# Performance work log

Hardware: AMD Instinct MI355X
Metric: run time of the kernel (lower is better)

## Reference

```python
import jax, jax.numpy as jnp
import numpy as np

B, T, C, D = 16, 2048, 1024, 64

def setup_inputs() -> dict:
    key = jax.random.key(0)
    kx, kq, kk, kv = jax.random.split(key, 4)
    x = jax.random.normal(kx, (B, T, C), dtype=jnp.float32)
    # nn.Linear(emb_size, head_size, bias=False): y = x @ W, store W as [C, D]
    s = 1.0 / np.sqrt(C)
    Wq = jax.random.normal(kq, (C, D), dtype=jnp.float32) * s
    Wk = jax.random.normal(kk, (C, D), dtype=jnp.float32) * s
    Wv = jax.random.normal(kv, (C, D), dtype=jnp.float32) * s
    return {"x": x, "Wq": Wq, "Wk": Wk, "Wv": Wv}

def reference(x, Wq, Wk, Wv):
    Bv, Tv, Cv = x.shape
    q = jnp.einsum('btc,cd->btd', x, Wq)
    k = jnp.einsum('btc,cd->btd', x, Wk)
    v = jnp.einsum('btc,cd->btd', x, Wv)
    # NOTE: original scales by C**0.5 (emb_size), not head_size**0.5
    scores = jnp.einsum('bqd,bkd->bqk', q, k) / jnp.sqrt(jnp.float32(Cv))
    causal = jnp.tril(jnp.ones((Tv, Tv), dtype=bool))
    scores = jnp.where(causal[None, :, :], scores, -jnp.inf)
    weights = jax.nn.softmax(scores, axis=-1)
    # dropout(p=0.4) omitted: reference assumes eval mode (identity)
    return jnp.einsum('bqk,bkd->bqd', weights, v)
```

## Files before the change

### kernel.cpp

```cpp
#include <hip/hip_runtime.h>
#include <math.h>


#define B_ 16
#define T_ 2048
#define C_ 1024
#define D_ 64
#define BT_ (B_ * T_)

typedef __attribute__((ext_vector_type(8))) short short8;
typedef __attribute__((ext_vector_type(4))) float f32x4;

__device__ __forceinline__ unsigned short f2bf(float f) {
    unsigned u = __float_as_uint(f);
    return (unsigned short)((u + 0x7fffu + ((u >> 16) & 1u)) >> 16);
}
__device__ __forceinline__ float bf2f(unsigned short h) {
    return __uint_as_float(((unsigned)h) << 16);
}
#define MFMA16(a, b, c) __builtin_amdgcn_mfma_f32_16x16x32_bf16((a), (b), (c), 0, 0, 0)

__global__ __launch_bounds__(256) void wprep_kernel(
    const float* __restrict__ Wq, const float* __restrict__ Wk,
    const float* __restrict__ Wv, short* __restrict__ WTh, short* __restrict__ WTl)
{
    int id = blockIdx.x * 256 + threadIdx.x;
    int n  = id >> 6;
    int c0 = (id & 63) << 4;
    const float* W = (n < 64) ? Wq : (n < 128) ? Wk : Wv;
    int d = n & 63;
    short8 h0, h1, l0, l1;
    #pragma unroll
    for (int i = 0; i < 8; ++i) {
        float w = W[(size_t)(c0 + i) * 64 + d];
        unsigned short hh = f2bf(w);
        h0[i] = (short)hh; l0[i] = (short)f2bf(w - bf2f(hh));
        float w2 = W[(size_t)(c0 + 8 + i) * 64 + d];
        unsigned short hh2 = f2bf(w2);
        h1[i] = (short)hh2; l1[i] = (short)f2bf(w2 - bf2f(hh2));
    }
    size_t o = (size_t)n * 1024 + c0;
    *(short8*)&WTh[o] = h0; *(short8*)&WTh[o + 8] = h1;
    *(short8*)&WTl[o] = l0; *(short8*)&WTl[o + 8] = l1;
}

__global__ __launch_bounds__(256) void qkv_mfma_kernel(
    const float* __restrict__ x, const short* __restrict__ WTh,
    const short* __restrict__ WTl, float* __restrict__ qf,
    short* __restrict__ kbf, short* __restrict__ vtb)
{
    __shared__ alignas(16) short xh[64 * 64];
    __shared__ alignas(16) short xl[64 * 64];

    const int tid = threadIdx.x;
    const int row0 = blockIdx.x * 64;
    const int lane = tid & 63, w = tid >> 6;
    const int lr = lane & 15, lg = lane >> 4;
    const int sr = tid >> 2, sc = (tid & 3) * 16;

    f32x4 acc[4][3];
    #pragma unroll
    for (int mt = 0; mt < 4; ++mt)
        #pragma unroll
        for (int gi = 0; gi < 3; ++gi) acc[mt][gi] = (f32x4){0.f, 0.f, 0.f, 0.f};

    for (int kb = 0; kb < C_; kb += 64) {
        float xv[16];
        const float* xp = &x[(size_t)(row0 + sr) * C_ + kb + sc];
        *(float4*)&xv[0]  = *(const float4*)&xp[0];
        *(float4*)&xv[4]  = *(const float4*)&xp[4];
        *(float4*)&xv[8]  = *(const float4*)&xp[8];
        *(float4*)&xv[12] = *(const float4*)&xp[12];
        short8 h0, h1, l0, l1;
        #pragma unroll
        for (int i = 0; i < 8; ++i) {
            unsigned short hh = f2bf(xv[i]);
            h0[i] = (short)hh; l0[i] = (short)f2bf(xv[i] - bf2f(hh));
            unsigned short hh2 = f2bf(xv[8 + i]);
            h1[i] = (short)hh2; l1[i] = (short)f2bf(xv[8 + i] - bf2f(hh2));
        }
        __syncthreads();
        {
            int u0 = (sc >> 3), u1 = u0 + 1;
            *(short8*)&xh[sr * 64 + (u0 ^ (sr & 7)) * 8] = h0;
            *(short8*)&xh[sr * 64 + (u1 ^ (sr & 7)) * 8] = h1;
            *(short8*)&xl[sr * 64 + (u0 ^ (sr & 7)) * 8] = l0;
            *(short8*)&xl[sr * 64 + (u1 ^ (sr & 7)) * 8] = l1;
        }
        __syncthreads();

        #pragma unroll
        for (int kc = 0; kc < 2; ++kc) {
            short8 ah[4], al[4];
            #pragma unroll
            for (int mt = 0; mt < 4; ++mt) {
                int r = mt * 16 + lr;
                int usw = (kc * 4 + lg) ^ (r & 7);
                ah[mt] = *(short8*)&xh[r * 64 + usw * 8];
                al[mt] = *(short8*)&xl[r * 64 + usw * 8];
            }
            #pragma unroll
            for (int gi = 0; gi < 3; ++gi) {
                int n = (3 * w + gi) * 16 + lr;
                size_t wo = (size_t)n * 1024 + kb + kc * 32 + lg * 8;
                short8 wh = *(const short8*)&WTh[wo];
                short8 wl = *(const short8*)&WTl[wo];
                #pragma unroll
                for (int mt = 0; mt < 4; ++mt) {
                    acc[mt][gi] = MFMA16(ah[mt], wh, acc[mt][gi]);
                    acc[mt][gi] = MFMA16(ah[mt], wl, acc[mt][gi]);
                    acc[mt][gi] = MFMA16(al[mt], wh, acc[mt][gi]);
                }
            }
        }
    }

    #pragma unroll
    for (int mt = 0; mt < 4; ++mt) {
        int rbase = row0 + mt * 16 + lg * 4;
        #pragma unroll
        for (int gi = 0; gi < 3; ++gi) {
            int g = 3 * w + gi;
            f32x4 a = acc[mt][gi];
            int col = g * 16 + lr;
            if (g < 4) {
                #pragma unroll
                for (int reg = 0; reg < 4; ++reg)
                    qf[(size_t)(rbase + reg) * 64 + col] = a[reg];
            } else if (g < 8) {
                #pragma unroll
                for (int reg = 0; reg < 4; ++reg)
                    kbf[(size_t)(rbase + reg) * 64 + (col - 64)] = (short)f2bf(a[reg]);
            } else {
                int d = col - 128;
                int bb = rbase >> 11, t0 = rbase & (T_ - 1);
                short4 pk;
                pk.x = (short)f2bf(a[0]); pk.y = (short)f2bf(a[1]);
                pk.z = (short)f2bf(a[2]); pk.w = (short)f2bf(a[3]);
                *(short4*)&vtb[((size_t)(bb * 64 + d) << 11) + t0] = pk;
            }
        }
    }
}

__global__ __launch_bounds__(256) void attn_mfma_kernel(
    const float* __restrict__ qf, const short* __restrict__ kbf,
    const short* __restrict__ vtb, float* __restrict__ out)
{
    __shared__ alignas(16) short kbuf[64 * 64];
    __shared__ alignas(16) short vbuf[64 * 64];
    __shared__ alignas(16) short pbuf[4 * 16 * 64];

    const int bid = blockIdx.x;
    const int b  = bid & 15;
    const int qt = 31 - (bid >> 4);
    const int tid = threadIdx.x;
    const int lane = tid & 63, w = tid >> 6;
    const int lr = lane & 15, lg = lane >> 4;
    const int qrow0 = qt * 64 + w * 16;
    const size_t base_tok = (size_t)b * T_;

    short8 qh[2], ql[2];
    #pragma unroll
    for (int kc = 0; kc < 2; ++kc) {
        const float* qp = &qf[(base_tok + qrow0 + lr) * 64 + kc * 32 + lg * 8];
        float4 q0 = *(const float4*)qp;
        float4 q1 = *(const float4*)(qp + 4);
        float qs[8] = {q0.x, q0.y, q0.z, q0.w, q1.x, q1.y, q1.z, q1.w};
        #pragma unroll
        for (int i = 0; i < 8; ++i) {
            float v = qs[i] * 0.03125f;
            unsigned short hh = f2bf(v);
            qh[kc][i] = (short)hh;
            ql[kc][i] = (short)f2bf(v - bf2f(hh));
        }
    }

    f32x4 o[4];
    #pragma unroll
    for (int dt = 0; dt < 4; ++dt) o[dt] = (f32x4){0.f, 0.f, 0.f, 0.f};
    float m[4]    = {-INFINITY, -INFINITY, -INFINITY, -INFINITY};
    float lsum[4] = {0.f, 0.f, 0.f, 0.f};

    const int sr = tid >> 2, su = tid & 3;
    const short* Kb = kbf + base_tok * 64;
    const short* Vb = vtb + (size_t)b * 64 * T_;

    int4 kreg[2], vreg[2];
    auto load_regs = [&](int jt) {
        int j0 = jt * 64;
        #pragma unroll
        for (int c = 0; c < 2; ++c) {
            kreg[c] = *(const int4*)&Kb[(size_t)(j0 + sr) * 64 + (su * 2 + c) * 8];
            vreg[c] = *(const int4*)&Vb[(size_t)sr * T_ + j0 + (su * 2 + c) * 8];
        }
    };
    auto write_bufs = [&]() {
        #pragma unroll
        for (int c = 0; c < 2; ++c) {
            int usw = (su * 2 + c) ^ (sr & 7);
            *(int4*)&kbuf[sr * 64 + usw * 8] = kreg[c];
            *(int4*)&vbuf[sr * 64 + usw * 8] = vreg[c];
        }
    };

    load_regs(0);
    write_bufs();
    __syncthreads();

    for (int jt = 0; jt <= qt; ++jt) {
        if (jt < qt) load_regs(jt + 1);

        f32x4 s[4];
        #pragma unroll
        for (int nt = 0; nt < 4; ++nt) s[nt] = (f32x4){0.f, 0.f, 0.f, 0.f};
        #pragma unroll
        for (int kc = 0; kc < 2; ++kc)
            #pragma unroll
            for (int nt = 0; nt < 4; ++nt) {
                int kj = nt * 16 + lr;
                int usw = (kc * 4 + lg) ^ (kj & 7);
                short8 kf = *(short8*)&kbuf[kj * 64 + usw * 8];
                s[nt] = MFMA16(qh[kc], kf, s[nt]);
                s[nt] = MFMA16(ql[kc], kf, s[nt]);
            }

        if (jt == qt) {
            int j0 = jt * 64;
            #pragma unroll
            for (int nt = 0; nt < 4; ++nt) {
                int j = j0 + nt * 16 + lr;
                #pragma unroll
                for (int reg = 0; reg < 4; ++reg)
                    if (j > qrow0 + lg * 4 + reg) s[nt][reg] = -INFINITY;
            }
        }

        float corr[4], psum[4] = {0.f, 0.f, 0.f, 0.f};
        #pragma unroll
        for (int reg = 0; reg < 4; ++reg) {
            float vmax = fmaxf(fmaxf(s[0][reg], s[1][reg]),
                               fmaxf(s[2][reg], s[3][reg]));
            vmax = fmaxf(vmax, __shfl_xor(vmax, 1));
            vmax = fmaxf(vmax, __shfl_xor(vmax, 2));
            vmax = fmaxf(vmax, __shfl_xor(vmax, 4));
            vmax = fmaxf(vmax, __shfl_xor(vmax, 8));
            float mnew = fmaxf(m[reg], vmax);
            corr[reg] = __expf(m[reg] - mnew);
            m[reg] = mnew;
        }
        #pragma unroll
        for (int nt = 0; nt < 4; ++nt)
            #pragma unroll
            for (int reg = 0; reg < 4; ++reg) {
                float p = __expf(s[nt][reg] - m[reg]);
                psum[reg] += p;
                int qr = lg * 4 + reg;
                int colj = nt * 16 + lr;
                int usw = (colj >> 3) ^ (qr & 7);
                pbuf[(w * 16 + qr) * 64 + usw * 8 + (colj & 7)] = (short)f2bf(p);
            }
        #pragma unroll
        for (int reg = 0; reg < 4; ++reg)
            lsum[reg] = lsum[reg] * corr[reg] + psum[reg];
        #pragma unroll
        for (int dt = 0; dt < 4; ++dt) {
            o[dt][0] *= corr[0]; o[dt][1] *= corr[1];
            o[dt][2] *= corr[2]; o[dt][3] *= corr[3];
        }

        asm volatile("s_waitcnt lgkmcnt(0)" ::: "memory");
        __builtin_amdgcn_sched_barrier(0);
        short8 pf[2];
        #pragma unroll
        for (int kc = 0; kc < 2; ++kc) {
            int usw = (kc * 4 + lg) ^ (lr & 7);
            pf[kc] = *(short8*)&pbuf[(w * 16 + lr) * 64 + usw * 8];
        }
        #pragma unroll
        for (int dt = 0; dt < 4; ++dt)
            #pragma unroll
            for (int kc = 0; kc < 2; ++kc) {
                int d = dt * 16 + lr;
                int usw = (kc * 4 + lg) ^ (d & 7);
                short8 vf = *(short8*)&vbuf[d * 64 + usw * 8];
                o[dt] = MFMA16(pf[kc], vf, o[dt]);
            }

        if (jt < qt) {
            __syncthreads();
            write_bufs();
            __syncthreads();
        }
    }

    #pragma unroll
    for (int reg = 0; reg < 4; ++reg) {
        lsum[reg] += __shfl_xor(lsum[reg], 1);
        lsum[reg] += __shfl_xor(lsum[reg], 2);
        lsum[reg] += __shfl_xor(lsum[reg], 4);
        lsum[reg] += __shfl_xor(lsum[reg], 8);
        lsum[reg] = 1.f / lsum[reg];
    }
    #pragma unroll
    for (int dt = 0; dt < 4; ++dt)
        #pragma unroll
        for (int reg = 0; reg < 4; ++reg)
            out[(base_tok + qrow0 + lg * 4 + reg) * 64 + dt * 16 + lr] =
                o[dt][reg] * lsum[reg];
}

extern "C" void kernel_launch(void* const* d_in, const int* in_sizes, int n_in,
                              void* d_out, int out_size, void* d_ws, size_t ws_size,
                              hipStream_t stream) {
    const float* x  = (const float*)d_in[0];
    const float* Wq = (const float*)d_in[1];
    const float* Wk = (const float*)d_in[2];
    const float* Wv = (const float*)d_in[3];
    float* out = (float*)d_out;

    float* qf  = (float*)d_ws;
    short* kbf = (short*)(qf + (size_t)BT_ * 64);
    short* vtb = kbf + (size_t)BT_ * 64;
    short* WTh = vtb + (size_t)BT_ * 64;
    short* WTl = WTh + (size_t)192 * 1024;

    wprep_kernel<<<48, 256, 0, stream>>>(Wq, Wk, Wv, WTh, WTl);
    qkv_mfma_kernel<<<512, 256, 0, stream>>>(x, WTh, WTl, qf, kbf, vtb);
    attn_mfma_kernel<<<512, 256, 0, stream>>>(qf, kbf, vtb, out);
}
```

Measured before the change: 315.9 us.

## Rebalance attention per-wave causal tiles, halve QKV block rows, tile weight prep

The attention kernel now gives each wave its own 16-row query tile. Waves pair short and long causal rows so work is balanced, and each wave reads K and V fragments directly from global memory into registers with K double-buffered. This removes the shared K/V staging and the block-wide barriers. The QKV projection uses 32-row blocks (1024 blocks) to raise occupancy, and weight prep transposes through shared memory for coalesced loads. The trade-off is more redundant global/L2 traffic for K/V, since each wave reads the same data separately, plus more register pressure.

Measured after the change: 326.8 us. 1.03x slower.

```diff
diff --git a/kernel.cpp b/kernel.cpp
--- a/kernel.cpp
+++ b/kernel.cpp
@@ -24,22 +24,29 @@
     const float* __restrict__ Wq, const float* __restrict__ Wk,
     const float* __restrict__ Wv, short* __restrict__ WTh, short* __restrict__ WTl)
 {
-    int id = blockIdx.x * 256 + threadIdx.x;
-    int n  = id >> 6;
-    int c0 = (id & 63) << 4;
-    const float* W = (n < 64) ? Wq : (n < 128) ? Wk : Wv;
-    int d = n & 63;
+    __shared__ float ws[64][65];
+    const int bid = blockIdx.x, tid = threadIdx.x;
+    const int wi = bid >> 4, ct = bid & 15, c0 = ct * 64;
+    const float* W = (wi == 0) ? Wq : (wi == 1) ? Wk : Wv;
+    #pragma unroll
+    for (int i = 0; i < 4; ++i) {
+        int rr = (tid >> 4) + i * 16;
+        int dd = (tid & 15) * 4;
+        *(float4*)&ws[rr][dd] = *(const float4*)&W[(size_t)(c0 + rr) * 64 + dd];
+    }
+    __syncthreads();
+    const int d = tid >> 2, cc0 = (tid & 3) * 16;
     short8 h0, h1, l0, l1;
     #pragma unroll
     for (int i = 0; i < 8; ++i) {
-        float w = W[(size_t)(c0 + i) * 64 + d];
-        unsigned short hh = f2bf(w);
-        h0[i] = (short)hh; l0[i] = (short)f2bf(w - bf2f(hh));
-        float w2 = W[(size_t)(c0 + 8 + i) * 64 + d];
-        unsigned short hh2 = f2bf(w2);
-        h1[i] = (short)hh2; l1[i] = (short)f2bf(w2 - bf2f(hh2));
-    }
-    size_t o = (size_t)n * 1024 + c0;
+        float v = ws[cc0 + i][d];
+        unsigned short hh = f2bf(v);
+        h0[i] = (short)hh; l0[i] = (short)f2bf(v - bf2f(hh));
+        float v2 = ws[cc0 + 8 + i][d];
+        unsigned short hh2 = f2bf(v2);
+        h1[i] = (short)hh2; l1[i] = (short)f2bf(v2 - bf2f(hh2));
+    }
+    size_t o = (size_t)(wi * 64 + d) * 1024 + c0 + cc0;
     *(short8*)&WTh[o] = h0; *(short8*)&WTh[o + 8] = h1;
     *(short8*)&WTl[o] = l0; *(short8*)&WTl[o + 8] = l1;
 }
@@ -49,51 +56,45 @@
     const short* __restrict__ WTl, float* __restrict__ qf,
     short* __restrict__ kbf, short* __restrict__ vtb)
 {
-    __shared__ alignas(16) short xh[64 * 64];
-    __shared__ alignas(16) short xl[64 * 64];
+    __shared__ alignas(16) short xh[32 * 64];
+    __shared__ alignas(16) short xl[32 * 64];
 
     const int tid = threadIdx.x;
-    const int row0 = blockIdx.x * 64;
+    const int row0 = blockIdx.x * 32;
     const int lane = tid & 63, w = tid >> 6;
     const int lr = lane & 15, lg = lane >> 4;
-    const int sr = tid >> 2, sc = (tid & 3) * 16;
-
-    f32x4 acc[4][3];
-    #pragma unroll
-    for (int mt = 0; mt < 4; ++mt)
+    const int sr = tid >> 3, sc = (tid & 7) * 8;
+
+    f32x4 acc[2][3];
+    #pragma unroll
+    for (int mt = 0; mt < 2; ++mt)
         #pragma unroll
         for (int gi = 0; gi < 3; ++gi) acc[mt][gi] = (f32x4){0.f, 0.f, 0.f, 0.f};
 
     for (int kb = 0; kb < C_; kb += 64) {
-        float xv[16];
+        float xv[8];
         const float* xp = &x[(size_t)(row0 + sr) * C_ + kb + sc];
-        *(float4*)&xv[0]  = *(const float4*)&xp[0];
-        *(float4*)&xv[4]  = *(const float4*)&xp[4];
-        *(float4*)&xv[8]  = *(const float4*)&xp[8];
-        *(float4*)&xv[12] = *(const float4*)&xp[12];
-        short8 h0, h1, l0, l1;
+        *(float4*)&xv[0] = *(const float4*)&xp[0];
+        *(float4*)&xv[4] = *(const float4*)&xp[4];
+        short8 h0, l0;
         #pragma unroll
         for (int i = 0; i < 8; ++i) {
             unsigned short hh = f2bf(xv[i]);
             h0[i] = (short)hh; l0[i] = (short)f2bf(xv[i] - bf2f(hh));
-            unsigned short hh2 = f2bf(xv[8 + i]);
-            h1[i] = (short)hh2; l1[i] = (short)f2bf(xv[8 + i] - bf2f(hh2));
         }
         __syncthreads();
         {
-            int u0 = (sc >> 3), u1 = u0 + 1;
-            *(short8*)&xh[sr * 64 + (u0 ^ (sr & 7)) * 8] = h0;
-            *(short8*)&xh[sr * 64 + (u1 ^ (sr & 7)) * 8] = h1;
-            *(short8*)&xl[sr * 64 + (u0 ^ (sr & 7)) * 8] = l0;
-            *(short8*)&xl[sr * 64 + (u1 ^ (sr & 7)) * 8] = l1;
+            int u0 = (sc >> 3) ^ (sr & 7);
+            *(short8*)&xh[sr * 64 + u0 * 8] = h0;
+            *(short8*)&xl[sr * 64 + u0 * 8] = l0;
         }
         __syncthreads();
 
         #pragma unroll
         for (int kc = 0; kc < 2; ++kc) {
-            short8 ah[4], al[4];
-            #pragma unroll
-            for (int mt = 0; mt < 4; ++mt) {
+            short8 ah[2], al[2];
+            #pragma unroll
+            for (int mt = 0; mt < 2; ++mt) {
                 int r = mt * 16 + lr;
                 int usw = (kc * 4 + lg) ^ (r & 7);
                 ah[mt] = *(short8*)&xh[r * 64 + usw * 8];
@@ -106,7 +107,7 @@
                 short8 wh = *(const short8*)&WTh[wo];
                 short8 wl = *(const short8*)&WTl[wo];
                 #pragma unroll
-                for (int mt = 0; mt < 4; ++mt) {
+                for (int mt = 0; mt < 2; ++mt) {
                     acc[mt][gi] = MFMA16(ah[mt], wh, acc[mt][gi]);
                     acc[mt][gi] = MFMA16(ah[mt], wl, acc[mt][gi]);
                     acc[mt][gi] = MFMA16(al[mt], wh, acc[mt][gi]);
@@ -116,7 +117,7 @@
     }
 
     #pragma unroll
-    for (int mt = 0; mt < 4; ++mt) {
+    for (int mt = 0; mt < 2; ++mt) {
         int rbase = row0 + mt * 16 + lg * 4;
         #pragma unroll
         for (int gi = 0; gi < 3; ++gi) {
@@ -147,23 +148,31 @@
     const float* __restrict__ qf, const short* __restrict__ kbf,
     const short* __restrict__ vtb, float* __restrict__ out)
 {
-    __shared__ alignas(16) short kbuf[64 * 64];
-    __shared__ alignas(16) short vbuf[64 * 64];
     __shared__ alignas(16) short pbuf[4 * 16 * 64];
 
     const int bid = blockIdx.x;
     const int b  = bid & 15;
-    const int qt = 31 - (bid >> 4);
+    const int pp = (bid >> 4) & 31;
+    const int sw = (bid >> 8) & 1;
     const int tid = threadIdx.x;
     const int lane = tid & 63, w = tid >> 6;
     const int lr = lane & 15, lg = lane >> 4;
-    const int qrow0 = qt * 64 + w * 16;
+
+    const int sel = w >> 1;
+    const int hv  = (w & 1) ^ sw;
+    const int t   = hv ? (127 - 2 * pp - sel) : (2 * pp + sel);
+    const int trow0 = t * 16;
+    const int njt = (t >> 2) + 1;
+
     const size_t base_tok = (size_t)b * T_;
+    const short* Kb = kbf + base_tok * 64;
+    const short* Vb = vtb + (size_t)b * 64 * T_;
+    short* pw = pbuf + w * 16 * 64;
 
     short8 qh[2], ql[2];
     #pragma unroll
     for (int kc = 0; kc < 2; ++kc) {
-        const float* qp = &qf[(base_tok + qrow0 + lr) * 64 + kc * 32 + lg * 8];
+        const float* qp = &qf[(base_tok + trow0 + lr) * 64 + kc * 32 + lg * 8];
         float4 q0 = *(const float4*)qp;
         float4 q1 = *(const float4*)(qp + 4);
         float qs[8] = {q0.x, q0.y, q0.z, q0.w, q1.x, q1.y, q1.z, q1.w};
@@ -182,65 +191,54 @@
     float m[4]    = {-INFINITY, -INFINITY, -INFINITY, -INFINITY};
     float lsum[4] = {0.f, 0.f, 0.f, 0.f};
 
-    const int sr = tid >> 2, su = tid & 3;
-    const short* Kb = kbf + base_tok * 64;
-    const short* Vb = vtb + (size_t)b * 64 * T_;
-
-    int4 kreg[2], vreg[2];
-    auto load_regs = [&](int jt) {
+    short8 kfA[2][4], kfB[2][4];
+    auto loadK = [&](short8 (&kf)[2][4], int jt) {
         int j0 = jt * 64;
         #pragma unroll
-        for (int c = 0; c < 2; ++c) {
-            kreg[c] = *(const int4*)&Kb[(size_t)(j0 + sr) * 64 + (su * 2 + c) * 8];
-            vreg[c] = *(const int4*)&Vb[(size_t)sr * T_ + j0 + (su * 2 + c) * 8];
-        }
+        for (int kc = 0; kc < 2; ++kc)
+            #pragma unroll
+            for (int nt = 0; nt < 4; ++nt)
+                kf[kc][nt] = *(const short8*)
+                    &Kb[(size_t)(j0 + nt * 16 + lr) * 64 + kc * 32 + lg * 8];
     };
-    auto write_bufs = [&]() {
-        #pragma unroll
-        for (int c = 0; c < 2; ++c) {
-            int usw = (su * 2 + c) ^ (sr & 7);
-            *(int4*)&kbuf[sr * 64 + usw * 8] = kreg[c];
-            *(int4*)&vbuf[sr * 64 + usw * 8] = vreg[c];
-        }
-    };
-
-    load_regs(0);
-    write_bufs();
-    __syncthreads();
-
-    for (int jt = 0; jt <= qt; ++jt) {
-        if (jt < qt) load_regs(jt + 1);
-
-        f32x4 s[4];
-        #pragma unroll
-        for (int nt = 0; nt < 4; ++nt) s[nt] = (f32x4){0.f, 0.f, 0.f, 0.f};
+
+    auto doTile = [&](short8 (&kf)[2][4], short8 (&kfn)[2][4], int jt) {
+        f32x4 sx[4];
+        #pragma unroll
+        for (int nt = 0; nt < 4; ++nt) sx[nt] = (f32x4){0.f, 0.f, 0.f, 0.f};
         #pragma unroll
         for (int kc = 0; kc < 2; ++kc)
             #pragma unroll
             for (int nt = 0; nt < 4; ++nt) {
-                int kj = nt * 16 + lr;
-                int usw = (kc * 4 + lg) ^ (kj & 7);
-                short8 kf = *(short8*)&kbuf[kj * 64 + usw * 8];
-                s[nt] = MFMA16(qh[kc], kf, s[nt]);
-                s[nt] = MFMA16(ql[kc], kf, s[nt]);
-            }
-
-        if (jt == qt) {
-            int j0 = jt * 64;
+                sx[nt] = MFMA16(qh[kc], kf[kc][nt], sx[nt]);
+                sx[nt] = MFMA16(ql[kc], kf[kc][nt], sx[nt]);
+            }
+
+        const int j0 = jt * 64;
+        short8 vf[4][2];
+        #pragma unroll
+        for (int dt = 0; dt < 4; ++dt)
+            #pragma unroll
+            for (int kc = 0; kc < 2; ++kc)
+                vf[dt][kc] = *(const short8*)
+                    &Vb[(size_t)(dt * 16 + lr) * T_ + j0 + kc * 32 + lg * 8];
+        if (jt + 1 < njt) loadK(kfn, jt + 1);
+
+        if (jt == njt - 1) {
             #pragma unroll
             for (int nt = 0; nt < 4; ++nt) {
                 int j = j0 + nt * 16 + lr;
                 #pragma unroll
                 for (int reg = 0; reg < 4; ++reg)
-                    if (j > qrow0 + lg * 4 + reg) s[nt][reg] = -INFINITY;
+                    if (j > trow0 + lg * 4 + reg) sx[nt][reg] = -INFINITY;
             }
         }
 
         float corr[4], psum[4] = {0.f, 0.f, 0.f, 0.f};
         #pragma unroll
         for (int reg = 0; reg < 4; ++reg) {
-            float vmax = fmaxf(fmaxf(s[0][reg], s[1][reg]),
-                               fmaxf(s[2][reg], s[3][reg]));
+            float vmax = fmaxf(fmaxf(sx[0][reg], sx[1][reg]),
+                               fmaxf(sx[2][reg], sx[3][reg]));
             vmax = fmaxf(vmax, __shfl_xor(vmax, 1));
             vmax = fmaxf(vmax, __shfl_xor(vmax, 2));
             vmax = fmaxf(vmax, __shfl_xor(vmax, 4));
@@ -253,12 +251,12 @@
         for (int nt = 0; nt < 4; ++nt)
             #pragma unroll
             for (int reg = 0; reg < 4; ++reg) {
-                float p = __expf(s[nt][reg] - m[reg]);
+                float p = __expf(sx[nt][reg] - m[reg]);
                 psum[reg] += p;
                 int qr = lg * 4 + reg;
                 int colj = nt * 16 + lr;
                 int usw = (colj >> 3) ^ (qr & 7);
-                pbuf[(w * 16 + qr) * 64 + usw * 8 + (colj & 7)] = (short)f2bf(p);
+                pw[qr * 64 + usw * 8 + (colj & 7)] = (short)f2bf(p);
             }
         #pragma unroll
         for (int reg = 0; reg < 4; ++reg)
@@ -275,23 +273,22 @@
         #pragma unroll
         for (int kc = 0; kc < 2; ++kc) {
             int usw = (kc * 4 + lg) ^ (lr & 7);
-            pf[kc] = *(short8*)&pbuf[(w * 16 + lr) * 64 + usw * 8];
+            pf[kc] = *(short8*)&pw[lr * 64 + usw * 8];
         }
         #pragma unroll
         for (int dt = 0; dt < 4; ++dt)
             #pragma unroll
-            for (int kc = 0; kc < 2; ++kc) {
-                int d = dt * 16 + lr;
-                int usw = (kc * 4 + lg) ^ (d & 7);
-                short8 vf = *(short8*)&vbuf[d * 64 + usw * 8];
-                o[dt] = MFMA16(pf[kc], vf, o[dt]);
-            }
-
-        if (jt < qt) {
-            __syncthreads();
-            write_bufs();
-            __syncthreads();
-        }
+            for (int kc = 0; kc < 2; ++kc)
+                o[dt] = MFMA16(pf[kc], vf[dt][kc], o[dt]);
+    };
+
+    loadK(kfA, 0);
+    int jt = 0;
+    while (true) {
+        doTile(kfA, kfB, jt);
+        if (++jt == njt) break;
+        doTile(kfB, kfA, jt);
+        if (++jt == njt) break;
     }
 
     #pragma unroll
@@ -306,7 +303,7 @@
     for (int dt = 0; dt < 4; ++dt)
         #pragma unroll
         for (int reg = 0; reg < 4; ++reg)
-            out[(base_tok + qrow0 + lg * 4 + reg) * 64 + dt * 16 + lr] =
+            out[(base_tok + trow0 + lg * 4 + reg) * 64 + dt * 16 + lr] =
                 o[dt][reg] * lsum[reg];
 }
 
@@ -326,6 +323,6 @@
     short* WTl = WTh + (size_t)192 * 1024;
 
     wprep_kernel<<<48, 256, 0, stream>>>(Wq, Wk, Wv, WTh, WTl);
-    qkv_mfma_kernel<<<512, 256, 0, stream>>>(x, WTh, WTl, qf, kbf, vtb);
+    qkv_mfma_kernel<<<1024, 256, 0, stream>>>(x, WTh, WTl, qf, kbf, vtb);
     attn_mfma_kernel<<<512, 256, 0, stream>>>(qf, kbf, vtb, out);
 }
```
